# Kernel tuning notes

Measured on AMD Instinct MI355X. Metric: run time of the kernel, lower is better.

Reference implementation:

```python
import jax, jax.numpy as jnp
import numpy as np

# LSNNParameters defaults (norse-style)
ALPHA = 100.0            # surrogate sharpness
DT = 1e-3
TAU_SYN_INV = 1.0 / 0.005   # 200
TAU_MEM_INV = 1.0 / 0.01    # 100
TAU_ADAPT_INV = 1.0 / 800.0
V_LEAK = 0.0
V_RESET = 0.0
BETA = 1.8
VTH = 1.0                # sp.vth_init / v_th default


@jax.custom_vjp
def superspike(x):
    # Heaviside forward, SuperSpike surrogate backward ('super' method)
    return (x > 0).astype(x.dtype)

def _ss_fwd(x):
    return superspike(x), x

def _ss_bwd(x, g):
    return (g / (ALPHA * jnp.abs(x) + 1.0) ** 2,)

superspike.defvjp(_ss_fwd, _ss_bwd)


def lsnn_scan(x, w_in, w_rec):
    # x: [T, B, N_in]; w_in: [H, N_in]; w_rec: [H, H]
    T, B, _ = x.shape
    H = w_in.shape[0]
    z0 = jnp.zeros((B, H), x.dtype)
    v0 = jnp.full((B, H), V_LEAK, x.dtype)
    i0 = jnp.zeros((B, H), x.dtype)
    b0 = jnp.full((B, H), VTH, x.dtype)  # mean(v_th)

    def step(carry, xt):
        z, v, i, b = carry
        v_dec = v + DT * TAU_MEM_INV * (V_LEAK - v + i)
        i_dec = i - DT * TAU_SYN_INV * i
        b_dec = b + DT * TAU_ADAPT_INV * (VTH - b)
        z_new = superspike(v_dec - b_dec)
        zd = jax.lax.stop_gradient(z_new)  # reset/adaptation use detached spike
        v_new = (1.0 - zd) * v_dec + zd * V_RESET
        i_new = i_dec + xt @ w_in.T + z @ w_rec.T
        b_new = b_dec + zd * BETA
        return (z_new, v_new, i_new, b_new), z_new

    (zf, vf, i_f, bf), outs = jax.lax.scan(step, (z0, v0, i0, b0), x)
    return outs, (zf, vf, i_f, bf)


def setup_inputs() -> dict:
    key = jax.random.key(0)
    k1, k2, k3 = jax.random.split(key, 3)
    T, B, N_IN, H = 512, 64, 512, 1024
    x = jax.random.normal(k1, (T, B, N_IN), jnp.float32)
    w_in = jax.random.normal(k2, (H, N_IN), jnp.float32) * np.float32(np.sqrt(2.0 / H))
    w_rec = jax.random.normal(k3, (H, H), jnp.float32) * np.float32(np.sqrt(2.0 / H))
    w_rec = w_rec * (1.0 - jnp.eye(H, dtype=jnp.float32))  # autapses=False
    return {"input_tensor": x, "input_weights": w_in, "recurrent_weights": w_rec}


def reference(input_tensor, input_weights, recurrent_weights):
    return lsnn_scan(input_tensor, input_weights, recurrent_weights)
```

## Files before the change

### kernel.cpp

```cpp
#include <hip/hip_runtime.h>

typedef float f32x4 __attribute__((ext_vector_type(4)));

#define T_STEPS 512
#define BATCH   64
#define NIN     512
#define H       1024
#define BH      (BATCH * H)

__global__ void transpose1024(const float* __restrict__ in, float* __restrict__ out) {
    __shared__ float tile[32][33];
    const int tx = threadIdx.x, ty = threadIdx.y;
    const int xg = blockIdx.x * 32 + tx;
    const int ybase = blockIdx.y * 32;
#pragma unroll
    for (int r = 0; r < 32; r += 8)
        tile[ty + r][tx] = in[(size_t)(ybase + ty + r) * H + xg];
    __syncthreads();
    const int x2 = blockIdx.y * 32 + tx;
    const int y2base = blockIdx.x * 32;
#pragma unroll
    for (int r = 0; r < 32; r += 8)
        out[(size_t)(y2base + ty + r) * H + x2] = tile[tx][ty + r];
}

#define BM 128
#define BN 128
#define BK 16
#define LDSS 132

__global__ __launch_bounds__(256) void gemm_xwin(const float* __restrict__ x,
                                                 const float* __restrict__ w,
                                                 float* __restrict__ cur) {
    __shared__ __align__(16) float As[BK][LDSS];
    __shared__ __align__(16) float Bs[BK][LDSS];
    const int tid = threadIdx.x;
    const int tx = tid & 15, ty = tid >> 4;
    const int tx4 = tx * 4, ty4 = ty * 4;
    const int m0 = blockIdx.y * BM;
    const int n0 = blockIdx.x * BN;

    float acc[8][8];
#pragma unroll
    for (int i = 0; i < 8; ++i)
#pragma unroll
        for (int j = 0; j < 8; ++j) acc[i][j] = 0.0f;

    const int ar = tid >> 2;
    const int akc = (tid & 3) * 4;

    for (int k0 = 0; k0 < NIN; k0 += BK) {
        const float4 a0 = *reinterpret_cast<const float4*>(&x[(size_t)(m0 + ar) * NIN + k0 + akc]);
        const float4 a1 = *reinterpret_cast<const float4*>(&x[(size_t)(m0 + ar + 64) * NIN + k0 + akc]);
        const float4 b0 = *reinterpret_cast<const float4*>(&w[(size_t)(n0 + ar) * NIN + k0 + akc]);
        const float4 b1 = *reinterpret_cast<const float4*>(&w[(size_t)(n0 + ar + 64) * NIN + k0 + akc]);
        __syncthreads();
        As[akc + 0][ar] = a0.x; As[akc + 1][ar] = a0.y; As[akc + 2][ar] = a0.z; As[akc + 3][ar] = a0.w;
        As[akc + 0][ar + 64] = a1.x; As[akc + 1][ar + 64] = a1.y; As[akc + 2][ar + 64] = a1.z; As[akc + 3][ar + 64] = a1.w;
        Bs[akc + 0][ar] = b0.x; Bs[akc + 1][ar] = b0.y; Bs[akc + 2][ar] = b0.z; Bs[akc + 3][ar] = b0.w;
        Bs[akc + 0][ar + 64] = b1.x; Bs[akc + 1][ar + 64] = b1.y; Bs[akc + 2][ar + 64] = b1.z; Bs[akc + 3][ar + 64] = b1.w;
        __syncthreads();

#pragma unroll
        for (int kk = 0; kk < BK; ++kk) {
            const float4 av0 = *reinterpret_cast<const float4*>(&As[kk][ty4]);
            const float4 av1 = *reinterpret_cast<const float4*>(&As[kk][ty4 + 64]);
            const float4 bv0 = *reinterpret_cast<const float4*>(&Bs[kk][tx4]);
            const float4 bv1 = *reinterpret_cast<const float4*>(&Bs[kk][tx4 + 64]);
            const float ar_[8] = {av0.x, av0.y, av0.z, av0.w, av1.x, av1.y, av1.z, av1.w};
            const float br_[8] = {bv0.x, bv0.y, bv0.z, bv0.w, bv1.x, bv1.y, bv1.z, bv1.w};
#pragma unroll
            for (int i = 0; i < 8; ++i)
#pragma unroll
                for (int j = 0; j < 8; ++j)
                    acc[i][j] = fmaf(ar_[i], br_[j], acc[i][j]);
        }
    }

#pragma unroll
    for (int gi = 0; gi < 2; ++gi)
#pragma unroll
        for (int ii = 0; ii < 4; ++ii) {
            const int i = gi * 4 + ii;
            const int row = m0 + ty4 + ii + gi * 64;
            float* dst = &cur[(size_t)row * H + n0 + tx4];
            *reinterpret_cast<float4*>(dst)      = make_float4(acc[i][0], acc[i][1], acc[i][2], acc[i][3]);
            *reinterpret_cast<float4*>(dst + 64) = make_float4(acc[i][4], acc[i][5], acc[i][6], acc[i][7]);
        }
}

__global__ __launch_bounds__(256) void lsnn_scan_kernel(float* __restrict__ io,
                                                        const float* __restrict__ wrecT) {
    const int b = blockIdx.x;
    const int tid = threadIdx.x;
    const int wave = tid >> 6, lane = tid & 63;
    const int j0 = tid * 4;

    __shared__ __align__(16) int list[2][4][256];
    __shared__ __align__(16) int cnt[2][4];

    float sv0 = 0.f, sv1 = 0.f, sv2 = 0.f, sv3 = 0.f;
    float si0 = 0.f, si1 = 0.f, si2 = 0.f, si3 = 0.f;
    float sb0 = 1.f, sb1 = 1.f, sb2 = 1.f, sb3 = 1.f;
    float sz0 = 0.f, sz1 = 0.f, sz2 = 0.f, sz3 = 0.f;
    int p = 0;

    const float C_MEM = (float)(1e-3 * 100.0);
    const float C_SYN = (float)(1e-3 * 200.0);
    const float C_AD  = (float)(1e-3 * (1.0 / 800.0));
    const float BETA  = 1.8f;

    float* base = io + (size_t)b * H + j0;

    if (lane == 0) cnt[0][wave] = 0;
    asm volatile("s_waitcnt lgkmcnt(0)" ::: "memory");
    __builtin_amdgcn_s_barrier();

    f32x4 P0 = *reinterpret_cast<const f32x4*>(base + (size_t)0 * BH);
    f32x4 P1 = *reinterpret_cast<const f32x4*>(base + (size_t)1 * BH);
    f32x4 P2 = *reinterpret_cast<const f32x4*>(base + (size_t)2 * BH);
    f32x4 P3 = *reinterpret_cast<const f32x4*>(base + (size_t)3 * BH);
    f32x4 P4 = *reinterpret_cast<const f32x4*>(base + (size_t)4 * BH);
    f32x4 P5 = *reinterpret_cast<const f32x4*>(base + (size_t)5 * BH);
    f32x4 P6 = *reinterpret_cast<const f32x4*>(base + (size_t)6 * BH);
    f32x4 P7 = *reinterpret_cast<const f32x4*>(base + (size_t)7 * BH);

#define SCAN_STEP(T, CREG, PF)                                                \
  {                                                                           \
    const float cc0 = CREG.x, cc1 = CREG.y, cc2 = CREG.z, cc3 = CREG.w;       \
    const int4 cn = *reinterpret_cast<const int4*>(&cnt[p][0]);               \
    float r0 = 0.f, r1 = 0.f, r2 = 0.f, r3 = 0.f;                             \
    _Pragma("unroll")                                                         \
    for (int w = 0; w < 4; ++w) {                                             \
      const int nw = (w == 0) ? cn.x : (w == 1) ? cn.y : (w == 2) ? cn.z : cn.w; \
      const int* lst = &list[p][w][0];                                        \
      int a = 0;                                                              \
      for (; a + 8 <= nw; a += 8) {                                           \
        const int h0 = lst[a],     h1 = lst[a + 1];                           \
        const int h2 = lst[a + 2], h3 = lst[a + 3];                           \
        const int h4 = lst[a + 4], h5 = lst[a + 5];                           \
        const int h6 = lst[a + 6], h7 = lst[a + 7];                           \
        const f32x4 wa = *(const f32x4*)(wrecT + (size_t)h0 * H + j0);        \
        const f32x4 wb = *(const f32x4*)(wrecT + (size_t)h1 * H + j0);        \
        const f32x4 wc = *(const f32x4*)(wrecT + (size_t)h2 * H + j0);        \
        const f32x4 wd = *(const f32x4*)(wrecT + (size_t)h3 * H + j0);        \
        const f32x4 we = *(const f32x4*)(wrecT + (size_t)h4 * H + j0);        \
        const f32x4 wf = *(const f32x4*)(wrecT + (size_t)h5 * H + j0);        \
        const f32x4 wg = *(const f32x4*)(wrecT + (size_t)h6 * H + j0);        \
        const f32x4 wh = *(const f32x4*)(wrecT + (size_t)h7 * H + j0);        \
        r0 += wa.x; r1 += wa.y; r2 += wa.z; r3 += wa.w;                       \
        r0 += wb.x; r1 += wb.y; r2 += wb.z; r3 += wb.w;                       \
        r0 += wc.x; r1 += wc.y; r2 += wc.z; r3 += wc.w;                       \
        r0 += wd.x; r1 += wd.y; r2 += wd.z; r3 += wd.w;                       \
        r0 += we.x; r1 += we.y; r2 += we.z; r3 += we.w;                       \
        r0 += wf.x; r1 += wf.y; r2 += wf.z; r3 += wf.w;                       \
        r0 += wg.x; r1 += wg.y; r2 += wg.z; r3 += wg.w;                       \
        r0 += wh.x; r1 += wh.y; r2 += wh.z; r3 += wh.w;                       \
      }                                                                       \
      for (; a < nw; ++a) {                                                   \
        const int h = lst[a];                                                 \
        const f32x4 w4 = *(const f32x4*)(wrecT + (size_t)h * H + j0);         \
        r0 += w4.x; r1 += w4.y; r2 += w4.z; r3 += w4.w;                       \
      }                                                                       \
    }                                                                         \
    const float vd0 = sv0 + C_MEM * (0.0f - sv0 + si0);                       \
    const float vd1 = sv1 + C_MEM * (0.0f - sv1 + si1);                       \
    const float vd2 = sv2 + C_MEM * (0.0f - sv2 + si2);                       \
    const float vd3 = sv3 + C_MEM * (0.0f - sv3 + si3);                       \
    const float id0 = si0 - C_SYN * si0;                                      \
    const float id1 = si1 - C_SYN * si1;                                      \
    const float id2 = si2 - C_SYN * si2;                                      \
    const float id3 = si3 - C_SYN * si3;                                      \
    const float bd0 = sb0 + C_AD * (1.0f - sb0);                              \
    const float bd1 = sb1 + C_AD * (1.0f - sb1);                              \
    const float bd2 = sb2 + C_AD * (1.0f - sb2);                              \
    const float bd3 = sb3 + C_AD * (1.0f - sb3);                              \
    sz0 = ((vd0 - bd0) > 0.0f) ? 1.0f : 0.0f;                                 \
    sz1 = ((vd1 - bd1) > 0.0f) ? 1.0f : 0.0f;                                 \
    sz2 = ((vd2 - bd2) > 0.0f) ? 1.0f : 0.0f;                                 \
    sz3 = ((vd3 - bd3) > 0.0f) ? 1.0f : 0.0f;                                 \
    sv0 = (sz0 > 0.0f) ? 0.0f : vd0;                                          \
    sv1 = (sz1 > 0.0f) ? 0.0f : vd1;                                          \
    sv2 = (sz2 > 0.0f) ? 0.0f : vd2;                                          \
    sv3 = (sz3 > 0.0f) ? 0.0f : vd3;                                          \
    sb0 = (sz0 > 0.0f) ? (bd0 + BETA) : bd0;                                  \
    sb1 = (sz1 > 0.0f) ? (bd1 + BETA) : bd1;                                  \
    sb2 = (sz2 > 0.0f) ? (bd2 + BETA) : bd2;                                  \
    sb3 = (sz3 > 0.0f) ? (bd3 + BETA) : bd3;                                  \
    si0 = (id0 + cc0) + r0;                                                   \
    si1 = (id1 + cc1) + r1;                                                   \
    si2 = (id2 + cc2) + r2;                                                   \
    si3 = (id3 + cc3) + r3;                                                   \
    if (PF) {                                                                 \
           \
      if ((T) + 1 < T_STEPS) {                                                \
        const float* pb = base + (size_t)((T) + 1) * BH;                      \
        P0 = *(const f32x4*)(pb + (size_t)0 * BH);                            \
        P1 = *(const f32x4*)(pb + (size_t)1 * BH);                            \
        P2 = *(const f32x4*)(pb + (size_t)2 * BH);                            \
        P3 = *(const f32x4*)(pb + (size_t)3 * BH);                            \
        P4 = *(const f32x4*)(pb + (size_t)4 * BH);                            \
        P5 = *(const f32x4*)(pb + (size_t)5 * BH);                            \
        P6 = *(const f32x4*)(pb + (size_t)6 * BH);                            \
        P7 = *(const f32x4*)(pb + (size_t)7 * BH);                            \
      }                                                                       \
    }                                                                         \
    *reinterpret_cast<f32x4*>(base + (size_t)(T) * BH) =                      \
        (f32x4){sz0, sz1, sz2, sz3};                                          \
    const unsigned long long m0 = __ballot(sz0 > 0.0f);                       \
    const unsigned long long m1 = __ballot(sz1 > 0.0f);                       \
    const unsigned long long m2 = __ballot(sz2 > 0.0f);                       \
    const unsigned long long m3 = __ballot(sz3 > 0.0f);                       \
    unsigned pos = __builtin_amdgcn_mbcnt_hi((unsigned)(m0 >> 32),            \
                   __builtin_amdgcn_mbcnt_lo((unsigned)m0, 0u));              \
    pos = __builtin_amdgcn_mbcnt_hi((unsigned)(m1 >> 32),                     \
          __builtin_amdgcn_mbcnt_lo((unsigned)m1, pos));                      \
    pos = __builtin_amdgcn_mbcnt_hi((unsigned)(m2 >> 32),                     \
          __builtin_amdgcn_mbcnt_lo((unsigned)m2, pos));                      \
    pos = __builtin_amdgcn_mbcnt_hi((unsigned)(m3 >> 32),                     \
          __builtin_amdgcn_mbcnt_lo((unsigned)m3, pos));                      \
    int* dst = &list[p ^ 1][wave][0];                                         \
    if (sz0 > 0.0f) dst[pos++] = j0 + 0;                                      \
    if (sz1 > 0.0f) dst[pos++] = j0 + 1;                                      \
    if (sz2 > 0.0f) dst[pos++] = j0 + 2;                                      \
    if (sz3 > 0.0f) dst[pos++] = j0 + 3;                                      \
    if (lane == 0)                                                            \
      cnt[p ^ 1][wave] = __popcll(m0) + __popcll(m1) + __popcll(m2) + __popcll(m3); \
    asm volatile("s_waitcnt lgkmcnt(0)" ::: "memory");                        \
    __builtin_amdgcn_s_barrier();                                             \
    p ^= 1;                                                                   \
  }

    for (int t = 0; t < T_STEPS; t += 8) {
        SCAN_STEP(t,     P0, 0);
        SCAN_STEP(t + 1, P1, 0);
        SCAN_STEP(t + 2, P2, 0);
        SCAN_STEP(t + 3, P3, 0);
        SCAN_STEP(t + 4, P4, 0);
        SCAN_STEP(t + 5, P5, 0);
        SCAN_STEP(t + 6, P6, 0);
        SCAN_STEP(t + 7, P7, 1);
    }
#undef SCAN_STEP

    float* fo = io + (size_t)T_STEPS * BH + (size_t)b * H + j0;
    *reinterpret_cast<float4*>(fo)          = make_float4(sz0, sz1, sz2, sz3);
    *reinterpret_cast<float4*>(fo + BH)     = make_float4(sv0, sv1, sv2, sv3);
    *reinterpret_cast<float4*>(fo + 2 * BH) = make_float4(si0, si1, si2, si3);
    *reinterpret_cast<float4*>(fo + 3 * BH) = make_float4(sb0, sb1, sb2, sb3);
}

extern "C" void kernel_launch(void* const* d_in, const int* in_sizes, int n_in,
                              void* d_out, int out_size, void* d_ws, size_t ws_size,
                              hipStream_t stream) {
    const float* x     = (const float*)d_in[0];
    const float* w_in  = (const float*)d_in[1];
    const float* w_rec = (const float*)d_in[2];
    float* out   = (float*)d_out;
    float* wrecT = (float*)d_ws;

    transpose1024<<<dim3(H / 32, H / 32), dim3(32, 8), 0, stream>>>(w_rec, wrecT);
    gemm_xwin<<<dim3(H / BN, (T_STEPS * BATCH) / BM), 256, 0, stream>>>(x, w_in, out);
    lsnn_scan_kernel<<<BATCH, 256, 0, stream>>>(out, wrecT);
}
```

Baseline: 827.9 us.

## Compact spike list and software-pipeline recurrent weight gathers across the scan step

Merges the four per-wave spike lists into one contiguous list using prefix offsets from the counts, which costs an extra barrier per step. Recurrent weight-row gathers are double-buffered in 16-row batches and issued before the state update. The tail is loaded as a masked batch and the list indices are made wave-uniform via readfirstlane. The intent is to hide global gather latency behind the elementwise update and the list build. In exchange it raises register pressure (48 f32x4 buffers, launch_bounds 256,1) and adds synchronisation.

Result: slower. 2.824 ms (+241.1%).

```diff
diff --git a/kernel.cpp b/kernel.cpp
--- a/kernel.cpp
+++ b/kernel.cpp
@@ -89,14 +89,14 @@
         }
 }
 
-__global__ __launch_bounds__(256) void lsnn_scan_kernel(float* __restrict__ io,
-                                                        const float* __restrict__ wrecT) {
+__global__ __launch_bounds__(256, 1) void lsnn_scan_kernel(float* __restrict__ io,
+                                                           const float* __restrict__ wrecT) {
     const int b = blockIdx.x;
     const int tid = threadIdx.x;
     const int wave = tid >> 6, lane = tid & 63;
     const int j0 = tid * 4;
 
-    __shared__ __align__(16) int list[2][4][256];
+    __shared__ __align__(16) int list[2][1024];
     __shared__ __align__(16) int cnt[2][4];
 
     float sv0 = 0.f, sv1 = 0.f, sv2 = 0.f, sv3 = 0.f;
@@ -125,44 +125,69 @@
     f32x4 P6 = *reinterpret_cast<const f32x4*>(base + (size_t)6 * BH);
     f32x4 P7 = *reinterpret_cast<const f32x4*>(base + (size_t)7 * BH);
 
+#define GLOAD(DST, IDX)                                                       \
+    DST = *reinterpret_cast<const f32x4*>(                                    \
+        wrecT + (size_t)(unsigned)__builtin_amdgcn_readfirstlane(IDX) * H + j0)
+
+#define LOAD16(BUF, A0)                                                       \
+  {                                                                           \
+    const int4 q0_ = *reinterpret_cast<const int4*>(lst + (A0));              \
+    const int4 q1_ = *reinterpret_cast<const int4*>(lst + (A0) + 4);          \
+    const int4 q2_ = *reinterpret_cast<const int4*>(lst + (A0) + 8);          \
+    const int4 q3_ = *reinterpret_cast<const int4*>(lst + (A0) + 12);         \
+    GLOAD(BUF[0],  q0_.x); GLOAD(BUF[1],  q0_.y);                             \
+    GLOAD(BUF[2],  q0_.z); GLOAD(BUF[3],  q0_.w);                             \
+    GLOAD(BUF[4],  q1_.x); GLOAD(BUF[5],  q1_.y);                             \
+    GLOAD(BUF[6],  q1_.z); GLOAD(BUF[7],  q1_.w);                             \
+    GLOAD(BUF[8],  q2_.x); GLOAD(BUF[9],  q2_.y);                             \
+    GLOAD(BUF[10], q2_.z); GLOAD(BUF[11], q2_.w);                             \
+    GLOAD(BUF[12], q3_.x); GLOAD(BUF[13], q3_.y);                             \
+    GLOAD(BUF[14], q3_.z); GLOAD(BUF[15], q3_.w);                             \
+  }
+
+#define ACC16(BUF)                                                            \
+  { _Pragma("unroll")                                                         \
+    for (int k_ = 0; k_ < 16; ++k_) {                                         \
+      r0 += BUF[k_].x; r1 += BUF[k_].y; r2 += BUF[k_].z; r3 += BUF[k_].w;     \
+    } }
+
+#define LOADT(BUF, A0)                                                        \
+  {                                                                           \
+    const int4 q0_ = *reinterpret_cast<const int4*>(lst + (A0));              \
+    const int4 q1_ = *reinterpret_cast<const int4*>(lst + (A0) + 4);          \
+    const int4 q2_ = *reinterpret_cast<const int4*>(lst + (A0) + 8);          \
+    const int4 q3_ = *reinterpret_cast<const int4*>(lst + (A0) + 12);         \
+    const int iv_[16] = {q0_.x, q0_.y, q0_.z, q0_.w, q1_.x, q1_.y, q1_.z,     \
+                         q1_.w, q2_.x, q2_.y, q2_.z, q2_.w, q3_.x, q3_.y,     \
+                         q3_.z, q3_.w};                                       \
+    _Pragma("unroll")                                                         \
+    for (int k_ = 0; k_ < 16; ++k_) {                                         \
+      const int h_ = ((A0) + k_ < n) ? iv_[k_] : 0;                           \
+      GLOAD(BUF[k_], h_);                                                     \
+    }                                                                         \
+  }
+
+#define ACCT(BUF, A0)                                                         \
+  { _Pragma("unroll")                                                         \
+    for (int k_ = 0; k_ < 16; ++k_) {                                         \
+      const float m_ = ((A0) + k_ < n) ? 1.0f : 0.0f;                         \
+      r0 = fmaf(m_, BUF[k_].x, r0); r1 = fmaf(m_, BUF[k_].y, r1);             \
+      r2 = fmaf(m_, BUF[k_].z, r2); r3 = fmaf(m_, BUF[k_].w, r3);             \
+    } }
+
 #define SCAN_STEP(T, CREG, PF)                                                \
   {                                                                           \
     const float cc0 = CREG.x, cc1 = CREG.y, cc2 = CREG.z, cc3 = CREG.w;       \
-    const int4 cn = *reinterpret_cast<const int4*>(&cnt[p][0]);               \
+    const int4 cq = *reinterpret_cast<const int4*>(&cnt[p][0]);               \
+    const int n = cq.x + cq.y + cq.z + cq.w;                                  \
+    const int nb = n >> 4;                                                    \
+    const int* lst = &list[p][0];                                             \
+    f32x4 gA[16], gB[16], gT[16];                                             \
     float r0 = 0.f, r1 = 0.f, r2 = 0.f, r3 = 0.f;                             \
-    _Pragma("unroll")                                                         \
-    for (int w = 0; w < 4; ++w) {                                             \
-      const int nw = (w == 0) ? cn.x : (w == 1) ? cn.y : (w == 2) ? cn.z : cn.w; \
-      const int* lst = &list[p][w][0];                                        \
-      int a = 0;                                                              \
-      for (; a + 8 <= nw; a += 8) {                                           \
-        const int h0 = lst[a],     h1 = lst[a + 1];                           \
-        const int h2 = lst[a + 2], h3 = lst[a + 3];                           \
-        const int h4 = lst[a + 4], h5 = lst[a + 5];                           \
-        const int h6 = lst[a + 6], h7 = lst[a + 7];                           \
-        const f32x4 wa = *(const f32x4*)(wrecT + (size_t)h0 * H + j0);        \
-        const f32x4 wb = *(const f32x4*)(wrecT + (size_t)h1 * H + j0);        \
-        const f32x4 wc = *(const f32x4*)(wrecT + (size_t)h2 * H + j0);        \
-        const f32x4 wd = *(const f32x4*)(wrecT + (size_t)h3 * H + j0);        \
-        const f32x4 we = *(const f32x4*)(wrecT + (size_t)h4 * H + j0);        \
-        const f32x4 wf = *(const f32x4*)(wrecT + (size_t)h5 * H + j0);        \
-        const f32x4 wg = *(const f32x4*)(wrecT + (size_t)h6 * H + j0);        \
-        const f32x4 wh = *(const f32x4*)(wrecT + (size_t)h7 * H + j0);        \
-        r0 += wa.x; r1 += wa.y; r2 += wa.z; r3 += wa.w;                       \
-        r0 += wb.x; r1 += wb.y; r2 += wb.z; r3 += wb.w;                       \
-        r0 += wc.x; r1 += wc.y; r2 += wc.z; r3 += wc.w;                       \
-        r0 += wd.x; r1 += wd.y; r2 += wd.z; r3 += wd.w;                       \
-        r0 += we.x; r1 += we.y; r2 += we.z; r3 += we.w;                       \
-        r0 += wf.x; r1 += wf.y; r2 += wf.z; r3 += wf.w;                       \
-        r0 += wg.x; r1 += wg.y; r2 += wg.z; r3 += wg.w;                       \
-        r0 += wh.x; r1 += wh.y; r2 += wh.z; r3 += wh.w;                       \
-      }                                                                       \
-      for (; a < nw; ++a) {                                                   \
-        const int h = lst[a];                                                 \
-        const f32x4 w4 = *(const f32x4*)(wrecT + (size_t)h * H + j0);         \
-        r0 += w4.x; r1 += w4.y; r2 += w4.z; r3 += w4.w;                       \
-      }                                                                       \
-    }                                                                         \
+                \
+    if (nb > 0) LOAD16(gA, 0);                                                \
+    if (nb > 1) LOAD16(gB, 16);                                               \
+                            \
     const float vd0 = sv0 + C_MEM * (0.0f - sv0 + si0);                       \
     const float vd1 = sv1 + C_MEM * (0.0f - sv1 + si1);                       \
     const float vd2 = sv2 + C_MEM * (0.0f - sv2 + si2);                       \
@@ -187,12 +212,7 @@
     sb1 = (sz1 > 0.0f) ? (bd1 + BETA) : bd1;                                  \
     sb2 = (sz2 > 0.0f) ? (bd2 + BETA) : bd2;                                  \
     sb3 = (sz3 > 0.0f) ? (bd3 + BETA) : bd3;                                  \
-    si0 = (id0 + cc0) + r0;                                                   \
-    si1 = (id1 + cc1) + r1;                                                   \
-    si2 = (id2 + cc2) + r2;                                                   \
-    si3 = (id3 + cc3) + r3;                                                   \
     if (PF) {                                                                 \
-           \
       if ((T) + 1 < T_STEPS) {                                                \
         const float* pb = base + (size_t)((T) + 1) * BH;                      \
         P0 = *(const f32x4*)(pb + (size_t)0 * BH);                            \
@@ -219,15 +239,42 @@
           __builtin_amdgcn_mbcnt_lo((unsigned)m2, pos));                      \
     pos = __builtin_amdgcn_mbcnt_hi((unsigned)(m3 >> 32),                     \
           __builtin_amdgcn_mbcnt_lo((unsigned)m3, pos));                      \
-    int* dst = &list[p ^ 1][wave][0];                                         \
+    if (lane == 0)                                                            \
+      cnt[p ^ 1][wave] = __popcll(m0) + __popcll(m1) + __popcll(m2) + __popcll(m3); \
+    asm volatile("s_waitcnt lgkmcnt(0)" ::: "memory");                        \
+    __builtin_amdgcn_s_barrier();                                             \
+                     \
+    const int4 nc = *reinterpret_cast<const int4*>(&cnt[p ^ 1][0]);           \
+    const int woff = (wave > 0 ? nc.x : 0) + (wave > 1 ? nc.y : 0) +          \
+                     (wave > 2 ? nc.z : 0);                                   \
+    int* dst = &list[p ^ 1][woff];                                            \
     if (sz0 > 0.0f) dst[pos++] = j0 + 0;                                      \
     if (sz1 > 0.0f) dst[pos++] = j0 + 1;                                      \
     if (sz2 > 0.0f) dst[pos++] = j0 + 2;                                      \
     if (sz3 > 0.0f) dst[pos++] = j0 + 3;                                      \
-    if (lane == 0)                                                            \
-      cnt[p ^ 1][wave] = __popcll(m0) + __popcll(m1) + __popcll(m2) + __popcll(m3); \
     asm volatile("s_waitcnt lgkmcnt(0)" ::: "memory");                        \
     __builtin_amdgcn_s_barrier();                                             \
+             \
+    if (n & 15) LOADT(gT, nb << 4);                                           \
+                \
+    int a = 32;                                                               \
+    bool useA = true;                                                         \
+    for (int i = 2; i < nb; ++i) {                                            \
+      if (useA) { ACC16(gA); LOAD16(gA, a); }                                 \
+      else      { ACC16(gB); LOAD16(gB, a); }                                 \
+      a += 16; useA = !useA;                                                  \
+    }                                                                         \
+    if (nb > 1) {                                                             \
+      if (useA) { ACC16(gA); ACC16(gB); }                                     \
+      else      { ACC16(gB); ACC16(gA); }                                     \
+    } else if (nb == 1) {                                                     \
+      ACC16(gA);                                                              \
+    }                                                                         \
+    if (n & 15) ACCT(gT, nb << 4);                                            \
+    si0 = (id0 + cc0) + r0;                                                   \
+    si1 = (id1 + cc1) + r1;                                                   \
+    si2 = (id2 + cc2) + r2;                                                   \
+    si3 = (id3 + cc3) + r3;                                                   \
     p ^= 1;                                                                   \
   }
 
@@ -242,6 +289,11 @@
         SCAN_STEP(t + 7, P7, 1);
     }
 #undef SCAN_STEP
+#undef ACCT
+#undef LOADT
+#undef ACC16
+#undef LOAD16
+#undef GLOAD
 
     float* fo = io + (size_t)T_STEPS * BH + (size_t)b * H + j0;
     *reinterpret_cast<float4*>(fo)          = make_float4(sz0, sz1, sz2, sz3);
```

## Fuse input GEMM and recurrent scan into one kernel with sentinel-based spin waits

Applied to the files above, without the earlier changes.

Merges the input-projection GEMM and the sequential LSNN scan into one launch. The first 64 blocks run the scan and the rest compute GEMM tiles. The output is pre-filled with a sentinel pattern via memset, and scan blocks spin with agent-scope atomic loads until the needed timesteps have real values. The goal is to overlap the GEMM with the latency-bound scan and remove the launch boundary. In exchange it adds a full-buffer memset, scalar atomic stores and loads in place of vector ones, and a dependence on the GEMM blocks being scheduled, with a bounded spin that could read a stale sentinel.

Result: slower. 880.2 us (+6.3%).

```diff
diff --git a/kernel.cpp b/kernel.cpp
--- a/kernel.cpp
+++ b/kernel.cpp
@@ -7,6 +7,21 @@
 #define NIN     512
 #define H       1024
 #define BH      (BATCH * H)
+#define SENTU   0x7F7F7F7Fu
+
+#define BM 128
+#define BN 128
+#define BK 16
+#define LDSS 132
+#define SCAN_BLOCKS 64
+#define GEMM_BLOCKS ((T_STEPS * BATCH / BM) * (H / BN))
+
+__device__ __forceinline__ float ld_agent(const float* p) {
+    return __hip_atomic_load(p, __ATOMIC_RELAXED, __HIP_MEMORY_SCOPE_AGENT);
+}
+__device__ __forceinline__ void st_agent(float* p, float v) {
+    __hip_atomic_store(p, v, __ATOMIC_RELAXED, __HIP_MEMORY_SCOPE_AGENT);
+}
 
 __global__ void transpose1024(const float* __restrict__ in, float* __restrict__ out) {
     __shared__ float tile[32][33];
@@ -24,80 +39,84 @@
         out[(size_t)(y2base + ty + r) * H + x2] = tile[tx][ty + r];
 }
 
-#define BM 128
-#define BN 128
-#define BK 16
-#define LDSS 132
-
-__global__ __launch_bounds__(256) void gemm_xwin(const float* __restrict__ x,
-                                                 const float* __restrict__ w,
-                                                 float* __restrict__ cur) {
-    __shared__ __align__(16) float As[BK][LDSS];
-    __shared__ __align__(16) float Bs[BK][LDSS];
-    const int tid = threadIdx.x;
-    const int tx = tid & 15, ty = tid >> 4;
-    const int tx4 = tx * 4, ty4 = ty * 4;
-    const int m0 = blockIdx.y * BM;
-    const int n0 = blockIdx.x * BN;
-
-    float acc[8][8];
-#pragma unroll
-    for (int i = 0; i < 8; ++i)
-#pragma unroll
-        for (int j = 0; j < 8; ++j) acc[i][j] = 0.0f;
-
-    const int ar = tid >> 2;
-    const int akc = (tid & 3) * 4;
-
-    for (int k0 = 0; k0 < NIN; k0 += BK) {
-        const float4 a0 = *reinterpret_cast<const float4*>(&x[(size_t)(m0 + ar) * NIN + k0 + akc]);
-        const float4 a1 = *reinterpret_cast<const float4*>(&x[(size_t)(m0 + ar + 64) * NIN + k0 + akc]);
-        const float4 b0 = *reinterpret_cast<const float4*>(&w[(size_t)(n0 + ar) * NIN + k0 + akc]);
-        const float4 b1 = *reinterpret_cast<const float4*>(&w[(size_t)(n0 + ar + 64) * NIN + k0 + akc]);
-        __syncthreads();
-        As[akc + 0][ar] = a0.x; As[akc + 1][ar] = a0.y; As[akc + 2][ar] = a0.z; As[akc + 3][ar] = a0.w;
-        As[akc + 0][ar + 64] = a1.x; As[akc + 1][ar + 64] = a1.y; As[akc + 2][ar + 64] = a1.z; As[akc + 3][ar + 64] = a1.w;
-        Bs[akc + 0][ar] = b0.x; Bs[akc + 1][ar] = b0.y; Bs[akc + 2][ar] = b0.z; Bs[akc + 3][ar] = b0.w;
-        Bs[akc + 0][ar + 64] = b1.x; Bs[akc + 1][ar + 64] = b1.y; Bs[akc + 2][ar + 64] = b1.z; Bs[akc + 3][ar + 64] = b1.w;
-        __syncthreads();
-
-#pragma unroll
-        for (int kk = 0; kk < BK; ++kk) {
-            const float4 av0 = *reinterpret_cast<const float4*>(&As[kk][ty4]);
-            const float4 av1 = *reinterpret_cast<const float4*>(&As[kk][ty4 + 64]);
-            const float4 bv0 = *reinterpret_cast<const float4*>(&Bs[kk][tx4]);
-            const float4 bv1 = *reinterpret_cast<const float4*>(&Bs[kk][tx4 + 64]);
-            const float ar_[8] = {av0.x, av0.y, av0.z, av0.w, av1.x, av1.y, av1.z, av1.w};
-            const float br_[8] = {bv0.x, bv0.y, bv0.z, bv0.w, bv1.x, bv1.y, bv1.z, bv1.w};
-#pragma unroll
-            for (int i = 0; i < 8; ++i)
-#pragma unroll
-                for (int j = 0; j < 8; ++j)
-                    acc[i][j] = fmaf(ar_[i], br_[j], acc[i][j]);
+__global__ void fused_gemm_scan(const float* __restrict__ x,
+                                const float* __restrict__ w,
+                                float* __restrict__ io,
+                                const float* __restrict__ wrecT) {
+    __shared__ __align__(16) char smem[2 * BK * LDSS * sizeof(float)];
+
+    if (blockIdx.x >= SCAN_BLOCKS) {
+        float* cur = io;
+        const int g = blockIdx.x - SCAN_BLOCKS;
+        const int m0 = (g >> 3) * BM;
+        const int n0 = (g & 7) * BN;
+
+        float (*As)[LDSS] = reinterpret_cast<float (*)[LDSS]>(smem);
+        float (*Bs)[LDSS] = reinterpret_cast<float (*)[LDSS]>(smem + BK * LDSS * sizeof(float));
+
+        const int tid = threadIdx.x;
+        const int tx = tid & 15, ty = tid >> 4;
+        const int tx4 = tx * 4, ty4 = ty * 4;
+
+        float acc[8][8];
+#pragma unroll
+        for (int i = 0; i < 8; ++i)
+#pragma unroll
+            for (int j = 0; j < 8; ++j) acc[i][j] = 0.0f;
+
+        const int ar = tid >> 2;
+        const int akc = (tid & 3) * 4;
+
+        for (int k0 = 0; k0 < NIN; k0 += BK) {
+            const float4 a0 = *reinterpret_cast<const float4*>(&x[(size_t)(m0 + ar) * NIN + k0 + akc]);
+            const float4 a1 = *reinterpret_cast<const float4*>(&x[(size_t)(m0 + ar + 64) * NIN + k0 + akc]);
+            const float4 b0 = *reinterpret_cast<const float4*>(&w[(size_t)(n0 + ar) * NIN + k0 + akc]);
+            const float4 b1 = *reinterpret_cast<const float4*>(&w[(size_t)(n0 + ar + 64) * NIN + k0 + akc]);
+            __syncthreads();
+            As[akc + 0][ar] = a0.x; As[akc + 1][ar] = a0.y; As[akc + 2][ar] = a0.z; As[akc + 3][ar] = a0.w;
+            As[akc + 0][ar + 64] = a1.x; As[akc + 1][ar + 64] = a1.y; As[akc + 2][ar + 64] = a1.z; As[akc + 3][ar + 64] = a1.w;
+            Bs[akc + 0][ar] = b0.x; Bs[akc + 1][ar] = b0.y; Bs[akc + 2][ar] = b0.z; Bs[akc + 3][ar] = b0.w;
+            Bs[akc + 0][ar + 64] = b1.x; Bs[akc + 1][ar + 64] = b1.y; Bs[akc + 2][ar + 64] = b1.z; Bs[akc + 3][ar + 64] = b1.w;
+            __syncthreads();
+
+#pragma unroll
+            for (int kk = 0; kk < BK; ++kk) {
+                const float4 av0 = *reinterpret_cast<const float4*>(&As[kk][ty4]);
+                const float4 av1 = *reinterpret_cast<const float4*>(&As[kk][ty4 + 64]);
+                const float4 bv0 = *reinterpret_cast<const float4*>(&Bs[kk][tx4]);
+                const float4 bv1 = *reinterpret_cast<const float4*>(&Bs[kk][tx4 + 64]);
+                const float ar_[8] = {av0.x, av0.y, av0.z, av0.w, av1.x, av1.y, av1.z, av1.w};
+                const float br_[8] = {bv0.x, bv0.y, bv0.z, bv0.w, bv1.x, bv1.y, bv1.z, bv1.w};
+#pragma unroll
+                for (int i = 0; i < 8; ++i)
+#pragma unroll
+                    for (int j = 0; j < 8; ++j)
+                        acc[i][j] = fmaf(ar_[i], br_[j], acc[i][j]);
+            }
         }
+
+#pragma unroll
+        for (int gi = 0; gi < 2; ++gi)
+#pragma unroll
+            for (int ii = 0; ii < 4; ++ii) {
+                const int i = gi * 4 + ii;
+                const int row = m0 + ty4 + ii + gi * 64;
+                float* dst = &cur[(size_t)row * H + n0 + tx4];
+                st_agent(dst + 0,  acc[i][0]); st_agent(dst + 1,  acc[i][1]);
+                st_agent(dst + 2,  acc[i][2]); st_agent(dst + 3,  acc[i][3]);
+                st_agent(dst + 64, acc[i][4]); st_agent(dst + 65, acc[i][5]);
+                st_agent(dst + 66, acc[i][6]); st_agent(dst + 67, acc[i][7]);
+            }
+        return;
     }
 
-#pragma unroll
-    for (int gi = 0; gi < 2; ++gi)
-#pragma unroll
-        for (int ii = 0; ii < 4; ++ii) {
-            const int i = gi * 4 + ii;
-            const int row = m0 + ty4 + ii + gi * 64;
-            float* dst = &cur[(size_t)row * H + n0 + tx4];
-            *reinterpret_cast<float4*>(dst)      = make_float4(acc[i][0], acc[i][1], acc[i][2], acc[i][3]);
-            *reinterpret_cast<float4*>(dst + 64) = make_float4(acc[i][4], acc[i][5], acc[i][6], acc[i][7]);
-        }
-}
-
-__global__ __launch_bounds__(256) void lsnn_scan_kernel(float* __restrict__ io,
-                                                        const float* __restrict__ wrecT) {
     const int b = blockIdx.x;
     const int tid = threadIdx.x;
     const int wave = tid >> 6, lane = tid & 63;
     const int j0 = tid * 4;
 
-    __shared__ __align__(16) int list[2][4][256];
-    __shared__ __align__(16) int cnt[2][4];
+    int (*list)[4][256] = reinterpret_cast<int (*)[4][256]>(smem);
+    int (*cnt)[4]       = reinterpret_cast<int (*)[4]>(smem + 8192);
 
     float sv0 = 0.f, sv1 = 0.f, sv2 = 0.f, sv3 = 0.f;
     float si0 = 0.f, si1 = 0.f, si2 = 0.f, si3 = 0.f;
@@ -116,14 +135,29 @@
     asm volatile("s_waitcnt lgkmcnt(0)" ::: "memory");
     __builtin_amdgcn_s_barrier();
 
-    f32x4 P0 = *reinterpret_cast<const f32x4*>(base + (size_t)0 * BH);
-    f32x4 P1 = *reinterpret_cast<const f32x4*>(base + (size_t)1 * BH);
-    f32x4 P2 = *reinterpret_cast<const f32x4*>(base + (size_t)2 * BH);
-    f32x4 P3 = *reinterpret_cast<const f32x4*>(base + (size_t)3 * BH);
-    f32x4 P4 = *reinterpret_cast<const f32x4*>(base + (size_t)4 * BH);
-    f32x4 P5 = *reinterpret_cast<const f32x4*>(base + (size_t)5 * BH);
-    f32x4 P6 = *reinterpret_cast<const f32x4*>(base + (size_t)6 * BH);
-    f32x4 P7 = *reinterpret_cast<const f32x4*>(base + (size_t)7 * BH);
+    f32x4 P0, P1, P2, P3, P4, P5, P6, P7;
+
+#define LDP(REG, KK)                                                          \
+      REG.x = ld_agent(pb_ + (size_t)(KK) * BH + 0);                          \
+      REG.y = ld_agent(pb_ + (size_t)(KK) * BH + 1);                          \
+      REG.z = ld_agent(pb_ + (size_t)(KK) * BH + 2);                          \
+      REG.w = ld_agent(pb_ + (size_t)(KK) * BH + 3);                          \
+      bad_ |= (unsigned)(__float_as_uint(REG.x) == SENTU);                    \
+      bad_ |= (unsigned)(__float_as_uint(REG.y) == SENTU);                    \
+      bad_ |= (unsigned)(__float_as_uint(REG.z) == SENTU);                    \
+      bad_ |= (unsigned)(__float_as_uint(REG.w) == SENTU);
+
+#define LOADP8_SPIN(PBASE)                                                    \
+  { const float* pb_ = (PBASE);                                               \
+    for (int tries_ = 0; tries_ < (1 << 14); ++tries_) {                      \
+      unsigned bad_ = 0u;                                                     \
+      LDP(P0, 0) LDP(P1, 1) LDP(P2, 2) LDP(P3, 3)                             \
+      LDP(P4, 4) LDP(P5, 5) LDP(P6, 6) LDP(P7, 7)                             \
+      if (__ballot(bad_ != 0u) == 0ull) break;                                \
+      __builtin_amdgcn_s_sleep(8);                                            \
+    } }
+
+    LOADP8_SPIN(base);
 
 #define SCAN_STEP(T, CREG, PF)                                                \
   {                                                                           \
@@ -192,17 +226,9 @@
     si2 = (id2 + cc2) + r2;                                                   \
     si3 = (id3 + cc3) + r3;                                                   \
     if (PF) {                                                                 \
-           \
+                    \
       if ((T) + 1 < T_STEPS) {                                                \
-        const float* pb = base + (size_t)((T) + 1) * BH;                      \
-        P0 = *(const f32x4*)(pb + (size_t)0 * BH);                            \
-        P1 = *(const f32x4*)(pb + (size_t)1 * BH);                            \
-        P2 = *(const f32x4*)(pb + (size_t)2 * BH);                            \
-        P3 = *(const f32x4*)(pb + (size_t)3 * BH);                            \
-        P4 = *(const f32x4*)(pb + (size_t)4 * BH);                            \
-        P5 = *(const f32x4*)(pb + (size_t)5 * BH);                            \
-        P6 = *(const f32x4*)(pb + (size_t)6 * BH);                            \
-        P7 = *(const f32x4*)(pb + (size_t)7 * BH);                            \
+        LOADP8_SPIN(base + (size_t)((T) + 1) * BH);                           \
       }                                                                       \
     }                                                                         \
     *reinterpret_cast<f32x4*>(base + (size_t)(T) * BH) =                      \
@@ -242,6 +268,8 @@
         SCAN_STEP(t + 7, P7, 1);
     }
 #undef SCAN_STEP
+#undef LOADP8_SPIN
+#undef LDP
 
     float* fo = io + (size_t)T_STEPS * BH + (size_t)b * H + j0;
     *reinterpret_cast<float4*>(fo)          = make_float4(sz0, sz1, sz2, sz3);
@@ -259,7 +287,7 @@
     float* out   = (float*)d_out;
     float* wrecT = (float*)d_ws;
 
+    hipMemsetAsync(out, 0x7F, (size_t)T_STEPS * BH * sizeof(float), stream);
     transpose1024<<<dim3(H / 32, H / 32), dim3(32, 8), 0, stream>>>(w_rec, wrecT);
-    gemm_xwin<<<dim3(H / BN, (T_STEPS * BATCH) / BM), 256, 0, stream>>>(x, w_in, out);
-    lsnn_scan_kernel<<<BATCH, 256, 0, stream>>>(out, wrecT);
-}
+    fused_gemm_scan<<<dim3(SCAN_BLOCKS + GEMM_BLOCKS), 256, 0, stream>>>(x, w_in, out, wrecT);
+}
```
